# Performance work log

Measured on AMD Instinct MI355X. Metric: run time of the kernel, lower is better.

## Reference

```python
import jax, jax.numpy as jnp
import numpy as np

NUM_HEADS = 8      # in_channels // num_head_channels = 512 // 64
NUM_GROUPS = 32    # GroupNorm groups
EPS = 1e-5


def setup_inputs() -> dict:
    key = jax.random.key(0)
    ks = jax.random.split(key, 6)
    C = 512
    x = jax.random.normal(ks[0], (8, C, 32, 32), dtype=jnp.float32)
    gn_w = jax.random.normal(ks[1], (C,), dtype=jnp.float32) * 0.1 + 1.0
    gn_b = jax.random.normal(ks[2], (C,), dtype=jnp.float32) * 0.1
    qkv_w = jax.random.normal(ks[3], (3 * C, C), dtype=jnp.float32) / np.sqrt(C)
    qkv_b = jnp.zeros((3 * C,), dtype=jnp.float32)
    # NOTE: original zero-initializes to_out; we use small random weights so the
    # attention path contributes to the output (math is identical).
    out_w = jax.random.normal(ks[4], (C, C), dtype=jnp.float32) * 0.02
    out_b = jax.random.normal(ks[5], (C,), dtype=jnp.float32) * 0.02
    return {"x": x, "gn_w": gn_w, "gn_b": gn_b, "qkv_w": qkv_w,
            "qkv_b": qkv_b, "out_w": out_w, "out_b": out_b}


def _group_norm(net, gn_w, gn_b):
    b, c, t = net.shape
    g = net.reshape(b, NUM_GROUPS, c // NUM_GROUPS, t)
    mu = jnp.mean(g, axis=(2, 3), keepdims=True)
    var = jnp.var(g, axis=(2, 3), keepdims=True)
    n = ((g - mu) * jax.lax.rsqrt(var + EPS)).reshape(b, c, t)
    return n * gn_w[None, :, None] + gn_b[None, :, None]


def reference(x, gn_w, gn_b, qkv_w, qkv_b, out_w, out_b):
    b, c, h, w = x.shape
    area = h * w
    inp = x.reshape(b, c, area)                      # [b, c, t]
    n = _group_norm(inp, gn_w, gn_b)
    # 1x1 conv1d == channel GEMM
    qkv = jnp.einsum('oc,bct->bot', qkv_w, n) + qkv_b[None, :, None]  # [b, 3c, t]
    hd = c // NUM_HEADS
    # split_qkv_after_heads: view(b*H, 3*hd, area) then split along channel
    qkv = qkv.reshape(b * NUM_HEADS, 3 * hd, area)
    q, k, v = qkv[:, :hd], qkv[:, hd:2 * hd], qkv[:, 2 * hd:]
    scale = 1.0 / np.sqrt(np.sqrt(hd))               # sqrt-sqrt per-tensor scale
    attn = jnp.einsum('bct,bcs->bts', q * scale, k * scale)  # [bH, t, s]
    prob = jax.nn.softmax(attn, axis=-1)
    net = jnp.einsum('bts,bcs->bct', prob, v).reshape(b, c, area)
    out = jnp.einsum('oc,bct->bot', out_w, net) + out_b[None, :, None]
    return (inp + out).reshape(b, c, h, w)
```

## Files before the change

kernel.cpp:

```cpp
#include <hip/hip_runtime.h>
#include <hip/hip_bf16.h>

typedef __bf16 bf16_t;
typedef __bf16 bf16x8 __attribute__((ext_vector_type(8)));
typedef __bf16 bf16x4 __attribute__((ext_vector_type(4)));
typedef short  s16x4  __attribute__((ext_vector_type(4)));
typedef float  f32x4  __attribute__((ext_vector_type(4)));

#define B_DIM 8
#define C_DIM 512
#define T_DIM 1024
#define NH 8
#define HD 64

#define QSCALE 0.180336880111112f

__device__ __forceinline__ f32x4 mfma16_bf16(bf16x4 a, bf16x4 b, f32x4 c) {
    return __builtin_amdgcn_mfma_f32_16x16x16bf16_1k(
        __builtin_bit_cast(s16x4, a), __builtin_bit_cast(s16x4, b), c, 0, 0, 0);
}

__device__ __forceinline__ void block_sync_lds() {
    asm volatile("s_waitcnt lgkmcnt(0)" ::: "memory");
    __builtin_amdgcn_s_barrier();
}

__global__ __launch_bounds__(256) void prep_w(const float* __restrict__ w1,
                                              const float* __restrict__ w2,
                                              bf16_t* __restrict__ o1,
                                              bf16_t* __restrict__ o2)
{
    int tid = blockIdx.x * 256 + threadIdx.x;
    for (int p = 0; p < 4; ++p) {
        int q = tid + p * 65536;
        const f32x4* src;
        bf16x4* dst;
        int qq;
        if (q < 196608) { src = (const f32x4*)w1; dst = (bf16x4*)o1; qq = q; }
        else            { src = (const f32x4*)w2; dst = (bf16x4*)o2; qq = q - 196608; }
        f32x4 f = src[qq];
        bf16x4 h;
        for (int j = 0; j < 4; ++j) h[j] = (bf16_t)f[j];
        dst[qq] = h;
    }
}

__global__ __launch_bounds__(256) void gn_kernel(const float* __restrict__ x,
                                                 const float* __restrict__ gw,
                                                 const float* __restrict__ gb,
                                                 bf16_t* __restrict__ n_t)
{
    __shared__ bf16_t sX[16384];
    __shared__ float sred[8];
    int tid = threadIdx.x;
    int bb  = blockIdx.x >> 5;
    int g   = blockIdx.x & 31;
    const f32x4* xg4 = reinterpret_cast<const f32x4*>(x + (size_t)(bb * C_DIM + g * 16) * T_DIM);

    float s = 0.f, sq = 0.f;
    for (int i = 0; i < 16; ++i) {
        int v = tid + i * 256;
        f32x4 f = xg4[v];
        bf16x4 h;
        for (int j = 0; j < 4; ++j) {
            s += f[j]; sq += f[j] * f[j];
            h[j] = (bf16_t)f[j];
        }
        *reinterpret_cast<bf16x4*>(sX + v * 4) = h;
    }
    for (int off = 1; off < 64; off <<= 1) {
        s  += __shfl_xor(s, off);
        sq += __shfl_xor(sq, off);
    }
    int wv = tid >> 6;
    if ((tid & 63) == 0) { sred[wv * 2] = s; sred[wv * 2 + 1] = sq; }
    __syncthreads();
    s  = sred[0] + sred[2] + sred[4] + sred[6];
    sq = sred[1] + sred[3] + sred[5] + sred[7];
    float mean = s * (1.f / 16384.f);
    float var  = sq * (1.f / 16384.f) - mean * mean;
    float rs   = rsqrtf(var + 1e-5f);

    int hf = tid & 1;
    float aa[8], bbias[8];
    for (int j = 0; j < 8; ++j) {
        int c = hf * 8 + j;
        float av = gw[g * 16 + c] * rs;
        aa[j] = av;
        bbias[j] = gb[g * 16 + c] - mean * av;
    }
    bf16_t* ob = n_t + (size_t)bb * T_DIM * C_DIM + g * 16 + hf * 8;
    for (int p = 0; p < 8; ++p) {
        int t = (tid >> 1) + p * 128;
        bf16x8 o;
        for (int j = 0; j < 8; ++j) {
            float xv = (float)sX[(hf * 8 + j) * 1024 + t];
            o[j] = (bf16_t)(xv * aa[j] + bbias[j]);
        }
        *reinterpret_cast<bf16x8*>(ob + (size_t)t * C_DIM) = o;
    }
}

__global__ __launch_bounds__(256) void qkv_gemm_kernel(
    const bf16_t* __restrict__ wqb, const float* __restrict__ bq,
    const bf16_t* __restrict__ n_t, bf16_t* __restrict__ qkv)
{
    __shared__ bf16_t sA[64 * 72];
    __shared__ bf16_t sB[128 * 72];
    int tid = threadIdx.x;
    int w = tid >> 6, lane = tid & 63, quad = lane >> 4, l15 = lane & 15;
    int bx = blockIdx.x;
    int t0 = blockIdx.y * 128;
    int bb = blockIdx.z;
    int o0 = bx * 64;
    const bf16_t* Ab = wqb + (size_t)o0 * C_DIM;
    const bf16_t* Bb = n_t + ((size_t)bb * T_DIM + t0) * C_DIM;

    f32x4 acc[2][4];
    for (int mt = 0; mt < 2; ++mt)
        for (int nt = 0; nt < 4; ++nt)
            acc[mt][nt] = f32x4{0.f, 0.f, 0.f, 0.f};
    int mw0 = (w >> 1) * 32;
    int nw0 = (w & 1) * 64;

    for (int k0 = 0; k0 < C_DIM; k0 += 64) {
        for (int i = 0; i < 2; ++i) {
            int v = tid + i * 256;
            int row = v >> 3, c8 = v & 7;
            *reinterpret_cast<bf16x8*>(sA + row * 72 + c8 * 8) =
                *reinterpret_cast<const bf16x8*>(Ab + (size_t)row * C_DIM + k0 + c8 * 8);
        }
        for (int i = 0; i < 4; ++i) {
            int v = tid + i * 256;
            int row = v >> 3, c8 = v & 7;
            *reinterpret_cast<bf16x8*>(sB + row * 72 + c8 * 8) =
                *reinterpret_cast<const bf16x8*>(Bb + (size_t)row * C_DIM + k0 + c8 * 8);
        }
        __syncthreads();
        for (int kk = 0; kk < 2; ++kk) {
            bf16x8 af[2], bfr[4];
            for (int mt = 0; mt < 2; ++mt)
                af[mt] = *reinterpret_cast<const bf16x8*>(sA + (mw0 + mt * 16 + l15) * 72 + kk * 32 + quad * 8);
            for (int nt = 0; nt < 4; ++nt)
                bfr[nt] = *reinterpret_cast<const bf16x8*>(sB + (nw0 + nt * 16 + l15) * 72 + kk * 32 + quad * 8);
            for (int mt = 0; mt < 2; ++mt)
                for (int nt = 0; nt < 4; ++nt)
                    acc[mt][nt] = __builtin_amdgcn_mfma_f32_16x16x32_bf16(af[mt], bfr[nt], acc[mt][nt], 0, 0, 0);
        }
        __syncthreads();
    }

    int h = bx / 3, type = bx % 3;
    size_t base = ((size_t)(bb * NH + h) * 3 + type) * (64 * 1024);

    if (type < 2) {
        float scl = (type == 0) ? QSCALE : 1.0f;
        for (int mt = 0; mt < 2; ++mt)
            for (int nt = 0; nt < 4; ++nt)
                for (int r = 0; r < 4; ++r) {
                    int mw = mw0 + mt * 16 + quad * 4 + r;
                    int tl = nw0 + nt * 16 + l15;
                    float v = (acc[mt][nt][r] + bq[o0 + mw]) * scl;
                    sB[tl * 72 + mw] = (bf16_t)v;
                }
        __syncthreads();
        for (int i = 0; i < 4; ++i) {
            int v = tid + i * 256;
            int tl = v >> 3, c8 = v & 7;
            bf16x8 d = *reinterpret_cast<const bf16x8*>(sB + tl * 72 + c8 * 8);
            *reinterpret_cast<bf16x8*>(qkv + base + (size_t)(t0 + tl) * 64 + c8 * 8) = d;
        }
    } else {
        for (int mt = 0; mt < 2; ++mt)
            for (int nt = 0; nt < 4; ++nt)
                for (int r = 0; r < 4; ++r) {
                    int mw = mw0 + mt * 16 + quad * 4 + r;
                    int tl = nw0 + nt * 16 + l15;
                    float v = acc[mt][nt][r] + bq[o0 + mw];
                    sB[mw * 136 + tl] = (bf16_t)v;
                }
        __syncthreads();
        for (int i = 0; i < 4; ++i) {
            int v = tid + i * 256;
            int cc = v >> 4, t8 = (v & 15) * 8;
            bf16x8 d = *reinterpret_cast<const bf16x8*>(sB + cc * 136 + t8);
            *reinterpret_cast<bf16x8*>(qkv + base + (size_t)cc * 1024 + t0 + t8) = d;
        }
    }
}

__global__ __launch_bounds__(256, 4) void attn_kernel(const bf16_t* __restrict__ qkv,
                                                      bf16_t* __restrict__ net_t)
{
    __shared__ bf16_t sK0[64 * 72];
    __shared__ bf16_t sV0[64 * 72];
    __shared__ bf16_t sK1[64 * 72];
    __shared__ bf16_t sV1[64 * 72];
    int tid = threadIdx.x;
    int w = tid >> 6, lane = tid & 63, quad = lane >> 4, l15 = lane & 15;
    int bh = blockIdx.x;
    int qt = blockIdx.y;
    size_t qb = (size_t)bh * 3 * 65536;
    const bf16_t* Qg = qkv + qb + (size_t)qt * 4096;
    const bf16_t* Kg = qkv + qb + 65536;
    const bf16_t* Vg = qkv + qb + 2 * 65536;

    bf16x8 qf[2];
    for (int kk = 0; kk < 2; ++kk)
        qf[kk] = *reinterpret_cast<const bf16x8*>(Qg + (size_t)(w * 16 + l15) * 64 + kk * 32 + quad * 8);

    int vrow = tid >> 3;
    int vcol = (tid & 7) * 8;

    bf16x8 kA[2], vA[2], kB[2], vB[2];

    auto load_tiles = [&](bf16x8* kr, bf16x8* vr, int s0) {
        for (int i = 0; i < 2; ++i) {
            int r = vrow + i * 32;
            kr[i] = *reinterpret_cast<const bf16x8*>(Kg + (size_t)(s0 + r) * 64 + vcol);
            vr[i] = *reinterpret_cast<const bf16x8*>(Vg + (size_t)r * 1024 + s0 + vcol);
        }
    };
    auto write_tiles = [&](bf16_t* sKb, bf16_t* sVb, const bf16x8* kr, const bf16x8* vr) {
        for (int i = 0; i < 2; ++i) {
            int r = vrow + i * 32;
            *reinterpret_cast<bf16x8*>(sKb + r * 72 + vcol) = kr[i];
            *reinterpret_cast<bf16x8*>(sVb + r * 72 + vcol) = vr[i];
        }
    };

    f32x4 O[4];
    for (int i = 0; i < 4; ++i) O[i] = f32x4{0.f, 0.f, 0.f, 0.f};
    f32x4 L = f32x4{0.f, 0.f, 0.f, 0.f};
    const bf16x4 kONES = bf16x4{(bf16_t)1.f, (bf16_t)1.f, (bf16_t)1.f, (bf16_t)1.f};

    auto compute_tile = [&](const bf16_t* sKb, const bf16_t* sVb) {
        __builtin_amdgcn_s_setprio(1);
        for (int mt = 0; mt < 4; ++mt) {
            f32x4 S = f32x4{0.f, 0.f, 0.f, 0.f};
            for (int kk = 0; kk < 2; ++kk) {
                bf16x8 kf = *reinterpret_cast<const bf16x8*>(sKb + (mt * 16 + l15) * 72 + kk * 32 + quad * 8);
                S = __builtin_amdgcn_mfma_f32_16x16x32_bf16(kf, qf[kk], S, 0, 0, 0);
            }
            bf16x4 pf;
            for (int r = 0; r < 4; ++r)
                pf[r] = (bf16_t)__builtin_amdgcn_exp2f(S[r]);
            L = mfma16_bf16(kONES, pf, L);
            for (int ct = 0; ct < 4; ++ct) {
                bf16x4 vf = *reinterpret_cast<const bf16x4*>(sVb + (ct * 16 + l15) * 72 + mt * 16 + quad * 4);
                O[ct] = mfma16_bf16(vf, pf, O[ct]);
            }
        }
        __builtin_amdgcn_s_setprio(0);
    };

    load_tiles(kA, vA, 0);
    write_tiles(sK0, sV0, kA, vA);
    load_tiles(kB, vB, 64);
    block_sync_lds();

    for (int st2 = 0; st2 < 8; ++st2) {
        write_tiles(sK1, sV1, kB, vB);
        if (st2 < 7) load_tiles(kA, vA, (2 * st2 + 2) * 64);
        compute_tile(sK0, sV0);
        block_sync_lds();
        if (st2 < 7) {
            write_tiles(sK0, sV0, kA, vA);
            load_tiles(kB, vB, (2 * st2 + 3) * 64);
        }
        compute_tile(sK1, sV1);
        if (st2 < 7) block_sync_lds();
    }

    float inv = 1.f / L[0];

    int bb = bh >> 3, h = bh & 7;
    int t = qt * 64 + w * 16 + l15;
    bf16_t* orow = net_t + ((size_t)bb * T_DIM + t) * C_DIM + h * 64;
    for (int ct = 0; ct < 4; ++ct) {
        bf16x4 o4;
        for (int r = 0; r < 4; ++r) o4[r] = (bf16_t)(O[ct][r] * inv);
        *reinterpret_cast<bf16x4*>(orow + ct * 16 + quad * 4) = o4;
    }
}

__global__ __launch_bounds__(256) void out_gemm_kernel(
    const bf16_t* __restrict__ wob, const float* __restrict__ bo,
    const bf16_t* __restrict__ net_t, const float* __restrict__ x,
    float* __restrict__ out)
{
    __shared__ bf16_t sA[64 * 72];
    __shared__ bf16_t sB[128 * 72];
    int tid = threadIdx.x;
    int w = tid >> 6, lane = tid & 63, quad = lane >> 4, l15 = lane & 15;
    int o0 = blockIdx.x * 64;
    int t0 = blockIdx.y * 128;
    int bb = blockIdx.z;
    const bf16_t* Ab = wob + (size_t)o0 * C_DIM;
    const bf16_t* Bb = net_t + ((size_t)bb * T_DIM + t0) * C_DIM;

    f32x4 acc[2][4];
    for (int mt = 0; mt < 2; ++mt)
        for (int nt = 0; nt < 4; ++nt)
            acc[mt][nt] = f32x4{0.f, 0.f, 0.f, 0.f};
    int mw0 = (w >> 1) * 32;
    int nw0 = (w & 1) * 64;

    for (int k0 = 0; k0 < C_DIM; k0 += 64) {
        for (int i = 0; i < 2; ++i) {
            int v = tid + i * 256;
            int row = v >> 3, c8 = v & 7;
            *reinterpret_cast<bf16x8*>(sA + row * 72 + c8 * 8) =
                *reinterpret_cast<const bf16x8*>(Ab + (size_t)row * C_DIM + k0 + c8 * 8);
        }
        for (int i = 0; i < 4; ++i) {
            int v = tid + i * 256;
            int row = v >> 3, c8 = v & 7;
            *reinterpret_cast<bf16x8*>(sB + row * 72 + c8 * 8) =
                *reinterpret_cast<const bf16x8*>(Bb + (size_t)row * C_DIM + k0 + c8 * 8);
        }
        __syncthreads();
        for (int kk = 0; kk < 2; ++kk) {
            bf16x8 af[2], bfr[4];
            for (int mt = 0; mt < 2; ++mt)
                af[mt] = *reinterpret_cast<const bf16x8*>(sA + (mw0 + mt * 16 + l15) * 72 + kk * 32 + quad * 8);
            for (int nt = 0; nt < 4; ++nt)
                bfr[nt] = *reinterpret_cast<const bf16x8*>(sB + (nw0 + nt * 16 + l15) * 72 + kk * 32 + quad * 8);
            for (int mt = 0; mt < 2; ++mt)
                for (int nt = 0; nt < 4; ++nt)
                    acc[mt][nt] = __builtin_amdgcn_mfma_f32_16x16x32_bf16(af[mt], bfr[nt], acc[mt][nt], 0, 0, 0);
        }
        __syncthreads();
    }

    for (int mt = 0; mt < 2; ++mt)
        for (int nt = 0; nt < 4; ++nt)
            for (int r = 0; r < 4; ++r) {
                int o = o0 + mw0 + mt * 16 + quad * 4 + r;
                int t = t0 + nw0 + nt * 16 + l15;
                size_t idx = ((size_t)bb * C_DIM + o) * T_DIM + t;
                out[idx] = acc[mt][nt][r] + bo[o] + x[idx];
            }
}

extern "C" void kernel_launch(void* const* d_in, const int* in_sizes, int n_in,
                              void* d_out, int out_size, void* d_ws, size_t ws_size,
                              hipStream_t stream)
{
    const float* x     = (const float*)d_in[0];
    const float* gn_w  = (const float*)d_in[1];
    const float* gn_b  = (const float*)d_in[2];
    const float* qkv_w = (const float*)d_in[3];
    const float* qkv_b = (const float*)d_in[4];
    const float* out_w = (const float*)d_in[5];
    const float* out_b = (const float*)d_in[6];
    float* out = (float*)d_out;

    char* ws = (char*)d_ws;
    bf16_t* n_t   = (bf16_t*)(ws);
    bf16_t* qkv   = (bf16_t*)(ws + 8388608);
    bf16_t* net_t = (bf16_t*)(ws + 33554432);
    bf16_t* wqb   = (bf16_t*)(ws + 41943040);
    bf16_t* wob   = (bf16_t*)(ws + 41943040 + 1572864);

    prep_w<<<dim3(256), 256, 0, stream>>>(qkv_w, out_w, wqb, wob);
    gn_kernel<<<dim3(256), 256, 0, stream>>>(x, gn_w, gn_b, n_t);
    qkv_gemm_kernel<<<dim3(24, 8, 8), 256, 0, stream>>>(wqb, qkv_b, n_t, qkv);
    attn_kernel<<<dim3(64, 16), 256, 0, stream>>>(qkv, net_t);
    out_gemm_kernel<<<dim3(8, 8, 8), 256, 0, stream>>>(wob, out_b, net_t, x, out);
}
```

Before: 157.1 us.

## Process two query tiles per attention block to reuse K/V tiles

Each attention block now handles 128 query rows (two 64-row tiles per wave) instead of 64, so every K/V tile staged in shared memory is reused for twice as many queries. The grid is halved to 512 blocks and the launch-bounds occupancy hint drops from 4 to 2 to leave room for the doubled accumulators. This is meant to cut global K/V loads and LDS fill traffic per query, in exchange for higher register pressure, fewer waves in flight to hide latency, and fewer blocks to spread across the GPU's compute units.

After: 152.9 us. -2.7%, faster.

```diff
diff --git a/kernel.cpp b/kernel.cpp
--- a/kernel.cpp
+++ b/kernel.cpp
@@ -189,7 +189,7 @@
     }
 }
 
-__global__ __launch_bounds__(256, 4) void attn_kernel(const bf16_t* __restrict__ qkv,
+__global__ __launch_bounds__(256, 2) void attn_kernel(const bf16_t* __restrict__ qkv,
                                                       bf16_t* __restrict__ net_t)
 {
     __shared__ bf16_t sK0[64 * 72];
@@ -201,13 +201,15 @@
     int bh = blockIdx.x;
     int qt = blockIdx.y;
     size_t qb = (size_t)bh * 3 * 65536;
-    const bf16_t* Qg = qkv + qb + (size_t)qt * 4096;
+    const bf16_t* Qg = qkv + qb + (size_t)qt * 8192;
     const bf16_t* Kg = qkv + qb + 65536;
     const bf16_t* Vg = qkv + qb + 2 * 65536;
 
-    bf16x8 qf[2];
-    for (int kk = 0; kk < 2; ++kk)
-        qf[kk] = *reinterpret_cast<const bf16x8*>(Qg + (size_t)(w * 16 + l15) * 64 + kk * 32 + quad * 8);
+    bf16x8 qf[2][2];
+    for (int tt = 0; tt < 2; ++tt)
+        for (int kk = 0; kk < 2; ++kk)
+            qf[tt][kk] = *reinterpret_cast<const bf16x8*>(
+                Qg + (size_t)(tt * 64 + w * 16 + l15) * 64 + kk * 32 + quad * 8);
 
     int vrow = tid >> 3;
     int vcol = (tid & 7) * 8;
@@ -229,26 +231,38 @@
         }
     };
 
-    f32x4 O[4];
-    for (int i = 0; i < 4; ++i) O[i] = f32x4{0.f, 0.f, 0.f, 0.f};
-    f32x4 L = f32x4{0.f, 0.f, 0.f, 0.f};
+    f32x4 O0[4], O1[4];
+    for (int i = 0; i < 4; ++i) {
+        O0[i] = f32x4{0.f, 0.f, 0.f, 0.f};
+        O1[i] = f32x4{0.f, 0.f, 0.f, 0.f};
+    }
+    f32x4 L0 = f32x4{0.f, 0.f, 0.f, 0.f};
+    f32x4 L1 = f32x4{0.f, 0.f, 0.f, 0.f};
     const bf16x4 kONES = bf16x4{(bf16_t)1.f, (bf16_t)1.f, (bf16_t)1.f, (bf16_t)1.f};
 
     auto compute_tile = [&](const bf16_t* sKb, const bf16_t* sVb) {
         __builtin_amdgcn_s_setprio(1);
         for (int mt = 0; mt < 4; ++mt) {
-            f32x4 S = f32x4{0.f, 0.f, 0.f, 0.f};
-            for (int kk = 0; kk < 2; ++kk) {
-                bf16x8 kf = *reinterpret_cast<const bf16x8*>(sKb + (mt * 16 + l15) * 72 + kk * 32 + quad * 8);
-                S = __builtin_amdgcn_mfma_f32_16x16x32_bf16(kf, qf[kk], S, 0, 0, 0);
+            const bf16_t* krow = sKb + (mt * 16 + l15) * 72 + quad * 8;
+            bf16x8 kf0 = *reinterpret_cast<const bf16x8*>(krow);
+            bf16x8 kf1 = *reinterpret_cast<const bf16x8*>(krow + 32);
+            f32x4 S0 = f32x4{0.f, 0.f, 0.f, 0.f};
+            f32x4 S1 = f32x4{0.f, 0.f, 0.f, 0.f};
+            S0 = __builtin_amdgcn_mfma_f32_16x16x32_bf16(kf0, qf[0][0], S0, 0, 0, 0);
+            S1 = __builtin_amdgcn_mfma_f32_16x16x32_bf16(kf0, qf[1][0], S1, 0, 0, 0);
+            S0 = __builtin_amdgcn_mfma_f32_16x16x32_bf16(kf1, qf[0][1], S0, 0, 0, 0);
+            S1 = __builtin_amdgcn_mfma_f32_16x16x32_bf16(kf1, qf[1][1], S1, 0, 0, 0);
+            bf16x4 pf0, pf1;
+            for (int r = 0; r < 4; ++r) {
+                pf0[r] = (bf16_t)__builtin_amdgcn_exp2f(S0[r]);
+                pf1[r] = (bf16_t)__builtin_amdgcn_exp2f(S1[r]);
             }
-            bf16x4 pf;
-            for (int r = 0; r < 4; ++r)
-                pf[r] = (bf16_t)__builtin_amdgcn_exp2f(S[r]);
-            L = mfma16_bf16(kONES, pf, L);
+            L0 = mfma16_bf16(kONES, pf0, L0);
+            L1 = mfma16_bf16(kONES, pf1, L1);
             for (int ct = 0; ct < 4; ++ct) {
                 bf16x4 vf = *reinterpret_cast<const bf16x4*>(sVb + (ct * 16 + l15) * 72 + mt * 16 + quad * 4);
-                O[ct] = mfma16_bf16(vf, pf, O[ct]);
+                O0[ct] = mfma16_bf16(vf, pf0, O0[ct]);
+                O1[ct] = mfma16_bf16(vf, pf1, O1[ct]);
             }
         }
         __builtin_amdgcn_s_setprio(0);
@@ -272,15 +286,21 @@
         if (st2 < 7) block_sync_lds();
     }
 
-    float inv = 1.f / L[0];
+    float inv0 = 1.f / L0[0];
+    float inv1 = 1.f / L1[0];
 
     int bb = bh >> 3, h = bh & 7;
-    int t = qt * 64 + w * 16 + l15;
-    bf16_t* orow = net_t + ((size_t)bb * T_DIM + t) * C_DIM + h * 64;
+    int tbase = qt * 128 + w * 16 + l15;
+    bf16_t* orow0 = net_t + ((size_t)bb * T_DIM + tbase) * C_DIM + h * 64;
+    bf16_t* orow1 = net_t + ((size_t)bb * T_DIM + tbase + 64) * C_DIM + h * 64;
     for (int ct = 0; ct < 4; ++ct) {
-        bf16x4 o4;
-        for (int r = 0; r < 4; ++r) o4[r] = (bf16_t)(O[ct][r] * inv);
-        *reinterpret_cast<bf16x4*>(orow + ct * 16 + quad * 4) = o4;
+        bf16x4 o4, o5;
+        for (int r = 0; r < 4; ++r) {
+            o4[r] = (bf16_t)(O0[ct][r] * inv0);
+            o5[r] = (bf16_t)(O1[ct][r] * inv1);
+        }
+        *reinterpret_cast<bf16x4*>(orow0 + ct * 16 + quad * 4) = o4;
+        *reinterpret_cast<bf16x4*>(orow1 + ct * 16 + quad * 4) = o5;
     }
 }
 
@@ -366,6 +386,6 @@
     prep_w<<<dim3(256), 256, 0, stream>>>(qkv_w, out_w, wqb, wob);
     gn_kernel<<<dim3(256), 256, 0, stream>>>(x, gn_w, gn_b, n_t);
     qkv_gemm_kernel<<<dim3(24, 8, 8), 256, 0, stream>>>(wqb, qkv_b, n_t, qkv);
-    attn_kernel<<<dim3(64, 16), 256, 0, stream>>>(qkv, net_t);
+    attn_kernel<<<dim3(64, 8), 256, 0, stream>>>(qkv, net_t);
     out_gemm_kernel<<<dim3(8, 8, 8), 256, 0, stream>>>(wob, out_b, net_t, x, out);
 }
```
